# Performance work log

Hardware: AMD Instinct MI355X
Metric: run time of the kernel (lower is better)

The kernel has to match this reference:

```python
import jax, jax.numpy as jnp
import numpy as np

EPS = 1e-10
BLOCK = 8


def _block_rfft2(x):
    # x: (N, 1, H, W) -> real/imag coeffs (N, K, 8, 5), matching torch.rfft(signal_ndim=2)/b**2
    N, C, H, W = x.shape
    b = BLOCK
    Hb, Wb = H // b, W // b
    # non-overlapping 8x8 blocks, row-major over (Hb, Wb) like nn.Unfold with stride=blocksize
    blocks = x[:, 0].reshape(N, Hb, b, Wb, b).transpose(0, 1, 3, 2, 4).reshape(N, Hb * Wb, b, b)
    c = jnp.fft.rfft2(blocks) / (b * b)  # (N, K, 8, 5) complex
    return jnp.real(c).astype(x.dtype), jnp.imag(c).astype(x.dtype)


def _soft_combine(a, b):
    # softmax-weighted blend of a and b along a virtual last axis (factor=1)
    stacked = jnp.stack([a, b], axis=-1)
    f = jax.nn.softmax(stacked, axis=-1)
    return a * f[..., 0] + b * f[..., 1]


def setup_inputs() -> dict:
    key = jax.random.key(0)
    k1, k2 = jax.random.split(key)
    N, H, W = 64, 512, 512
    inp = {
        "input": jax.random.normal(k1, (N, 1, H, W), dtype=jnp.float32),
        "target": jax.random.normal(k2, (N, 1, H, W), dtype=jnp.float32),
        # learned parameters at their init values (weight_size = (8, 5))
        "t_tild": jnp.zeros((BLOCK, BLOCK // 2 + 1), dtype=jnp.float32),
        "alpha": jnp.float32(0.1),
        "w_tild": jnp.float32(np.log(0.2 / 0.8)),
        "beta": jnp.float32(1.0),
        "w_phase_tild": jnp.zeros((BLOCK, BLOCK // 2 + 1), dtype=jnp.float32) - 2.0,
    }
    return inp


def reference(input, target, t_tild, alpha, w_tild, beta, w_phase_tild):
    # blockwise 2D rFFT of both images
    c0r, c0i = _block_rfft2(target)  # (N, K, 8, 5)
    c1r, c1i = _block_rfft2(input)

    # amplitude: frobenius norm over (real, imag) after +EPS, as in torch.norm(c0+EPS, dim=4)
    c0_amp = jnp.sqrt((c0r + EPS) ** 2 + (c0i + EPS) ** 2)
    c1_amp = jnp.sqrt((c1r + EPS) ** 2 + (c1i + EPS) ** 2)

    avg_lum = jnp.mean(c0_amp[:, :, 0, 0])
    t = jnp.exp(t_tild)  # (8, 5)
    lum = ((c0_amp[:, :, 0, 0] + EPS) / (avg_lum + EPS)) ** alpha  # (N, K)
    t_l = t[None, None, :, :] * lum[:, :, None, None]  # (N, K, 8, 5)

    w = jax.nn.sigmoid(w_tild)
    s = _soft_combine(t_l, (jnp.abs(c0_amp) + EPS) ** w * t_l ** (1 - w))

    # Watson amplitude distance (dropout in eval mode = identity)
    watson = (jnp.abs((c0_amp - c1_amp) / s) + EPS) ** beta + EPS
    watson = jnp.sum(watson, axis=(1, 2, 3)) ** (1.0 / beta)  # (N,)

    # phase distance
    c0_phase = jnp.arctan2(c0i, c0r + EPS)
    c1_phase = jnp.arctan2(c1i, c1r + EPS)
    w_phase = jnp.exp(w_phase_tild)  # trainable=True branch: no corner zeroing
    phase_dist = jnp.arccos(jnp.cos(c0_phase - c1_phase) * (1 - EPS * 1e3)) * w_phase
    phase_dist = jnp.sum(phase_dist, axis=(1, 2, 3))  # (N,)

    return watson + phase_dist  # reduction='none' -> (N,)
```

## Files before the change

kernel.cpp:

```cpp
#include <hip/hip_runtime.h>
#include <math.h>

#define EPSf 1e-10f
#define IMG_N 64
#define IMG_H 512
#define IMG_W 512
#define KBLK 4096
#define TOTAL_BLK (IMG_N * KBLK)
#define WG 256
#define NWG (TOTAL_BLK / WG)
#define NWG2 (TOTAL_BLK * 2 / WG)
#define CHUNKS 32

#define KCc 0.70710678118654752440f
#define SCc (1.0f / 64.0f)
#define LOG2E 1.44269504088896340736f

#define FSQRT(x) __builtin_amdgcn_sqrtf(x)
#define FRCP(x)  __builtin_amdgcn_rcpf(x)

__device__ __forceinline__ float dpp_xor1(float x) {
    int i = __builtin_bit_cast(int, x);
    i = __builtin_amdgcn_mov_dpp(i, 0xB1, 0xF, 0xF, true);
    return __builtin_bit_cast(float, i);
}

__device__ __forceinline__ float wave_red(float v) {
#pragma unroll
    for (int o = 32; o > 0; o >>= 1) v += __shfl_down(v, o, 64);
    return v;
}

__global__ __launch_bounds__(WG) void kA(const float* __restrict__ tgt,
                                         float* __restrict__ partA) {
    int gid = blockIdx.x * WG + threadIdx.x;
    int n = gid >> 12;
    int k = gid & 4095;
    int bi = k >> 6, bj = k & 63;
    const float* p = tgt + (size_t)n * (IMG_H * IMG_W) + (size_t)(bi * 8) * IMG_W + bj * 8;
    float s = 0.f;
#pragma unroll
    for (int r = 0; r < 8; r++) {
        float4 a = *(const float4*)(p + (size_t)r * IMG_W);
        float4 b = *(const float4*)(p + (size_t)r * IMG_W + 4);
        s += ((a.x + a.y) + (a.z + a.w)) + ((b.x + b.y) + (b.z + b.w));
    }
    float dc = s * (1.0f / 64.0f);
    float amp = sqrtf((dc + EPSf) * (dc + EPSf) + EPSf * EPSf);
    float wv = wave_red(amp);
    __shared__ float red[4];
    if ((threadIdx.x & 63) == 0) red[threadIdx.x >> 6] = wv;
    __syncthreads();
    if (threadIdx.x == 0) partA[blockIdx.x] = (red[0] + red[1]) + (red[2] + red[3]);
}

#define ROWFFT(A, B, P) do { \
    float s02 = (A).x + (B).x, d02 = (A).x - (B).x; \
    float s26 = (A).z + (B).z, d26 = (A).z - (B).z; \
    float s13 = (A).y + (B).y, d13 = (A).y - (B).y; \
    float s37 = (A).w + (B).w, d37 = (A).w - (B).w; \
    float e0 = s02 + s26, e2 = s02 - s26; \
    float o0 = s13 + s37, o2 = s13 - s37; \
    float cp = KCc * (d13 - d37), cm = KCc * (d13 + d37); \
    P##_0 = SCc * (e0 + o0);  P##_1 = SCc * (d02 + cp); \
    P##_2 = SCc * (-d26 - cm); P##_3 = SCc * e2; \
    P##_4 = SCc * (-o2);      P##_5 = SCc * (d02 - cp); \
    P##_6 = SCc * (d26 - cm); P##_7 = SCc * (e0 - o0); \
} while (0)

#define DECL8(P) float P##_0, P##_1, P##_2, P##_3, P##_4, P##_5, P##_6, P##_7

#define LOADROW(ptr, r, P) do { \
    float4 A = *(const float4*)((ptr) + (size_t)(r) * IMG_W); \
    float4 B = *(const float4*)((ptr) + (size_t)(r) * IMG_W + 4); \
    ROWFFT(A, B, P); \
} while (0)

#define CFFT8M(PFX, x0r,x0i,x1r,x1i,x2r,x2i,x3r,x3i,x4r,x4i,x5r,x5i,x6r,x6i,x7r,x7i) \
    float PFX##0r, PFX##0i, PFX##1r, PFX##1i, PFX##2r, PFX##2i, PFX##3r, PFX##3i, \
          PFX##4r, PFX##4i, PFX##5r, PFX##5i, PFX##6r, PFX##6i, PFX##7r, PFX##7i; \
    { \
        float t0r = (x0r) + (x4r), t0i = (x0i) + (x4i); \
        float t1r = (x0r) - (x4r), t1i = (x0i) - (x4i); \
        float t2r = (x2r) + (x6r), t2i = (x2i) + (x6i); \
        float t3r = (x2r) - (x6r), t3i = (x2i) - (x6i); \
        float E0r = t0r + t2r, E0i = t0i + t2i; \
        float E2r = t0r - t2r, E2i = t0i - t2i; \
        float E1r = t1r + t3i, E1i = t1i - t3r; \
        float E3r = t1r - t3i, E3i = t1i + t3r; \
        float u0r = (x1r) + (x5r), u0i = (x1i) + (x5i); \
        float u1r = (x1r) - (x5r), u1i = (x1i) - (x5i); \
        float u2r = (x3r) + (x7r), u2i = (x3i) + (x7i); \
        float u3r = (x3r) - (x7r), u3i = (x3i) - (x7i); \
        float O0r = u0r + u2r, O0i = u0i + u2i; \
        float O2r = u0r - u2r, O2i = u0i - u2i; \
        float O1r = u1r + u3i, O1i = u1i - u3r; \
        float O3r = u1r - u3i, O3i = u1i + u3r; \
        float W1r = KCc * (O1r + O1i), W1i = KCc * (O1i - O1r); \
        float W2r = O2i,               W2i = -O2r; \
        float W3r = KCc * (O3i - O3r), W3i = -KCc * (O3r + O3i); \
        PFX##0r = E0r + O0r; PFX##0i = E0i + O0i; \
        PFX##1r = E1r + W1r; PFX##1i = E1i + W1i; \
        PFX##2r = E2r + W2r; PFX##2i = E2i + W2i; \
        PFX##3r = E3r + W3r; PFX##3i = E3i + W3i; \
        PFX##4r = E0r - O0r; PFX##4i = E0i - O0i; \
        PFX##5r = E1r - W1r; PFX##5i = E1i - W1i; \
        PFX##6r = E2r - W2r; PFX##6i = E2i - W2i; \
        PFX##7r = E3r - W3r; PFX##7i = E3i - W3i; \
    }

__device__ __attribute__((noinline)) float2
coef2x2(float oRA, float oIA, float rRA, float rIA, float tA, float lA, float pA,
        float oRB, float oIB, float rRB, float rIB, float tB, float lB, float pB,
        float lum, float omw_llum, float w, float beta, int img, int b1i) {
    float oReA = oRA + EPSf, oIeA = oIA + EPSf;
    float rReA = rRA + EPSf, rIeA = rIA + EPSf;
    float oReB = oRB + EPSf, oIeB = oIB + EPSf;
    float rReB = rRB + EPSf, rIeB = rIB + EPSf;
    float aOA = FSQRT(fmaf(oReA, oReA, oIeA * oIeA));
    float aRA = FSQRT(fmaf(rReA, rReA, rIeA * rIeA));
    float aOB = FSQRT(fmaf(oReB, oReB, oIeB * oIeB));
    float aRB = FSQRT(fmaf(rReB, rReB, rIeB * rIeB));
    float a0A = img ? aRA : aOA;
    float a0B = img ? aRB : aOB;
    float dxA = fabsf(aOA - aRA);
    float dxB = fabsf(aOB - aRB);
    float l0A = __log2f(a0A + EPSf);
    float l0B = __log2f(a0B + EPSf);
    float bbA = exp2f(fmaf(w, l0A, lA + omw_llum));
    float bbB = exp2f(fmaf(w, l0B, lB + omw_llum));
    float tlA = tA * lum;
    float tlB = tB * lum;
    float eA = __expf(bbA - tlA);
    float eB = __expf(bbB - tlB);
    float xA = dxA * (1.f + eA) * FRCP(fmaf(bbA, eA, tlA));
    float xB = dxB * (1.f + eB) * FRCP(fmaf(bbB, eB, tlB));
    float dwA = b1i ? xA : (__powf(xA + EPSf, beta) + EPSf);
    float dwB = b1i ? xB : (__powf(xB + EPSf, beta) + EPSf);
    float dotA = fmaf(oReA, rReA, oIA * rIA);
    float dotB = fmaf(oReB, rReB, oIB * rIB);
    float cdA = dotA * FRCP(fmaxf(aOA * aRA, 1e-30f)) * (1.f - 1e-7f);
    float cdB = dotB * FRCP(fmaxf(aOB * aRB, 1e-30f)) * (1.f - 1e-7f);
    cdA = fminf(fmaxf(cdA, -1.f), 1.f);
    cdB = fminf(fmaxf(cdB, -1.f), 1.f);
    float tA2 = fabsf(cdA), tB2 = fabsf(cdB);
    float rA2 = FSQRT(1.f - tA2), rB2 = FSQRT(1.f - tB2);
    float plA = fmaf(fmaf(fmaf(-0.0187293f, tA2, 0.0742610f), tA2, -0.2121144f), tA2, 1.5707288f);
    float plB = fmaf(fmaf(fmaf(-0.0187293f, tB2, 0.0742610f), tB2, -0.2121144f), tB2, 1.5707288f);
    float acA = rA2 * plA;
    float acB = rB2 * plB;
    acA = (cdA < 0.f) ? (3.14159265358979f - acA) : acA;
    acB = (cdB < 0.f) ? (3.14159265358979f - acB) : acB;
    return make_float2(dwA + dwB, fmaf(acA, pA, acB * pB));
}

#define PAIRC2(QA, LAr, LAi, HAr, HAi, QB, LBr, LBi, HBr, HBi) do { \
    float sAr = img ? (LAr) : (HAr), sAi = img ? (LAi) : (HAi); \
    float rAr = dpp_xor1(sAr), rAi = dpp_xor1(sAi); \
    float oAr = img ? (HAr) : (LAr), oAi = img ? (HAi) : (LAi); \
    float sBr = img ? (LBr) : (HBr), sBi = img ? (LBi) : (HBi); \
    float rBr = dpp_xor1(sBr), rBi = dpp_xor1(sBi); \
    float oBr = img ? (HBr) : (LBr), oBi = img ? (HBi) : (LBi); \
    float2 dwp = coef2x2(oAr, oAi, rAr, rAi, (QA).x, (QA).y, (QA).z, \
                         oBr, oBi, rBr, rBi, (QB).x, (QB).y, (QB).z, \
                         lum, omw_llum, w, beta, img, b1i); \
    sumW += dwp.x; sumP += dwp.y; \
} while (0)

#define PREFQ(V) \
    float4 q0 = tab4[base20 + 0 * 5 + (V)]; \
    float4 q1 = tab4[base20 + 1 * 5 + (V)]; \
    float4 q2 = tab4[base20 + 2 * 5 + (V)]; \
    float4 q3 = tab4[base20 + 3 * 5 + (V)];

#define COEFS2() do { \
    PAIRC2(q0, X0r, X0i, X4r, X4i, q1, X1r, X1i, X5r, X5i); \
    PAIRC2(q2, X2r, X2i, X6r, X6i, q3, X3r, X3i, X7r, X7i); \
} while (0)

__global__ __launch_bounds__(WG, 4) void kC(const float* __restrict__ tgt,
                                            const float* __restrict__ inp,
                                            const float* __restrict__ t_tild,
                                            const float* __restrict__ alphaP,
                                            const float* __restrict__ wtP,
                                            const float* __restrict__ betaP,
                                            const float* __restrict__ wptP,
                                            const float* __restrict__ partA,
                                            float* __restrict__ partW,
                                            float* __restrict__ partP) {
    __shared__ float4 tab4[40];
    __shared__ float redA[4];
    float w = 1.f / (1.f + __expf(-wtP[0]));
    if (threadIdx.x < 40) {
        float tt = t_tild[threadIdx.x];
        tab4[threadIdx.x] = make_float4(__expf(tt), (1.f - w) * tt * LOG2E,
                                        __expf(wptP[threadIdx.x]), 0.f);
    }
    {
        float v = partA[threadIdx.x] + partA[threadIdx.x + 256] +
                  partA[threadIdx.x + 512] + partA[threadIdx.x + 768];
        float wv = wave_red(v);
        if ((threadIdx.x & 63) == 0) redA[threadIdx.x >> 6] = wv;
    }
    __syncthreads();
    float avg = ((redA[0] + redA[1]) + (redA[2] + redA[3])) * (1.0f / (float)TOTAL_BLK);
    float alpha = alphaP[0];
    float beta = betaP[0];
    float lavg = __log2f(avg + EPSf);
    int b1i = (beta == 1.0f) ? 1 : 0;

    int gid = blockIdx.x * WG + threadIdx.x;
    int p = gid >> 1;
    int img = gid & 1;
    int base20 = img * 20;
    int n = p >> 12, k = p & 4095;
    int bi = k >> 6, bj = k & 63;
    size_t off = (size_t)n * (IMG_H * IMG_W) + (size_t)(bi * 8) * IMG_W + bj * 8;
    const float* src = (img ? inp : tgt) + off;

    DECL8(t0); DECL8(t1); DECL8(t2); DECL8(t3);
    DECL8(t4); DECL8(t5); DECL8(t6); DECL8(t7);
    LOADROW(src, 0, t0); LOADROW(src, 1, t1); LOADROW(src, 2, t2); LOADROW(src, 3, t3);
    LOADROW(src, 4, t4); LOADROW(src, 5, t5); LOADROW(src, 6, t6); LOADROW(src, 7, t7);

    float sumW = 0.f, sumP = 0.f;
    float lum = 0.f, omw_llum = 0.f;

    {
        PREFQ(0)
        CFFT8M(X, t0_0, 0.f, t1_0, 0.f, t2_0, 0.f, t3_0, 0.f,
                  t4_0, 0.f, t5_0, 0.f, t6_0, 0.f, t7_0, 0.f)
        float rr = X0r + EPSf, ii = X0i + EPSf;
        float myamp = FSQRT(fmaf(rr, rr, ii * ii));
        float oamp = dpp_xor1(myamp);
        float amp00 = img ? oamp : myamp;
        float llum = alpha * (__log2f(amp00 + EPSf) - lavg);
        lum = exp2f(llum);
        omw_llum = (1.f - w) * llum;
        COEFS2();
    }
    {
        PREFQ(1)
        CFFT8M(X, t0_1, t0_2, t1_1, t1_2, t2_1, t2_2, t3_1, t3_2,
                  t4_1, t4_2, t5_1, t5_2, t6_1, t6_2, t7_1, t7_2)
        COEFS2();
    }
    {
        PREFQ(2)
        CFFT8M(X, t0_3, t0_4, t1_3, t1_4, t2_3, t2_4, t3_3, t3_4,
                  t4_3, t4_4, t5_3, t5_4, t6_3, t6_4, t7_3, t7_4)
        COEFS2();
    }
    {
        PREFQ(3)
        CFFT8M(X, t0_5, t0_6, t1_5, t1_6, t2_5, t2_6, t3_5, t3_6,
                  t4_5, t4_6, t5_5, t5_6, t6_5, t6_6, t7_5, t7_6)
        COEFS2();
    }
    {
        PREFQ(4)
        CFFT8M(X, t0_7, 0.f, t1_7, 0.f, t2_7, 0.f, t3_7, 0.f,
                  t4_7, 0.f, t5_7, 0.f, t6_7, 0.f, t7_7, 0.f)
        COEFS2();
    }

    if (b1i) sumW += 20.f * 2.f * EPSf;

    float wW = wave_red(sumW);
    float wP = wave_red(sumP);
    __shared__ float redW[4], redP[4];
    if ((threadIdx.x & 63) == 0) { redW[threadIdx.x >> 6] = wW; redP[threadIdx.x >> 6] = wP; }
    __syncthreads();
    if (threadIdx.x == 0) {
        partW[blockIdx.x] = (redW[0] + redW[1]) + (redW[2] + redW[3]);
        partP[blockIdx.x] = (redP[0] + redP[1]) + (redP[2] + redP[3]);
    }
}

__global__ __launch_bounds__(64) void kD(const float* __restrict__ partW,
                                         const float* __restrict__ partP,
                                         const float* __restrict__ betaP,
                                         float* __restrict__ out) {
    int n = threadIdx.x;
    float sW = 0.f, sP = 0.f;
#pragma unroll
    for (int c = 0; c < CHUNKS; c++) {
        sW += partW[n * CHUNKS + c];
        sP += partP[n * CHUNKS + c];
    }
    float beta = betaP[0];
    float wat = (beta == 1.0f) ? sW : __powf(sW, 1.0f / beta);
    out[n] = wat + sP;
}

extern "C" void kernel_launch(void* const* d_in, const int* in_sizes, int n_in,
                              void* d_out, int out_size, void* d_ws, size_t ws_size,
                              hipStream_t stream) {
    const float* inp    = (const float*)d_in[0];
    const float* tgt    = (const float*)d_in[1];
    const float* t_tild = (const float*)d_in[2];
    const float* alphaP = (const float*)d_in[3];
    const float* wtP    = (const float*)d_in[4];
    const float* betaP  = (const float*)d_in[5];
    const float* wptP   = (const float*)d_in[6];
    float* out = (float*)d_out;
    float* ws = (float*)d_ws;
    float* partA = ws;
    float* partW = ws + 1056;
    float* partP = ws + 3104;

    hipLaunchKernelGGL(kA, dim3(NWG), dim3(WG), 0, stream, tgt, partA);
    hipLaunchKernelGGL(kC, dim3(NWG2), dim3(WG), 0, stream, tgt, inp, t_tild,
                       alphaP, wtP, betaP, wptP, partA, partW, partP);
    hipLaunchKernelGGL(kD, dim3(1), dim3(64), 0, stream, partW, partP, betaP, out);
}
```

Baseline: 45.85 us.

## Fuse final reduction into kC via last-block atomic counter, tweak occupancy and log

Removes the separate kD launch: kC blocks increment a global counter after writing partials, and the last block reduces the partials and writes the output. The counter is reset in kA. The amplitude log is now computed from the squared magnitude (half log2 of mag²), which drops the +EPS inside the log, and kC's launch bounds are raised to 5 waves per EU. The aim is to save a kernel launch and a little ALU work. In exchange it adds an atomic and a fence per block, and may increase register pressure or cause spills.

```diff
diff --git a/kernel.cpp b/kernel.cpp
--- a/kernel.cpp
+++ b/kernel.cpp
@@ -32,7 +32,9 @@
 }
 
 __global__ __launch_bounds__(WG) void kA(const float* __restrict__ tgt,
-                                         float* __restrict__ partA) {
+                                         float* __restrict__ partA,
+                                         unsigned int* __restrict__ cnt) {
+    if (blockIdx.x == 0 && threadIdx.x == 0) cnt[0] = 0u;
     int gid = blockIdx.x * WG + threadIdx.x;
     int n = gid >> 12;
     int k = gid & 4095;
@@ -117,16 +119,16 @@
     float rReA = rRA + EPSf, rIeA = rIA + EPSf;
     float oReB = oRB + EPSf, oIeB = oIB + EPSf;
     float rReB = rRB + EPSf, rIeB = rIB + EPSf;
-    float aOA = FSQRT(fmaf(oReA, oReA, oIeA * oIeA));
-    float aRA = FSQRT(fmaf(rReA, rReA, rIeA * rIeA));
-    float aOB = FSQRT(fmaf(oReB, oReB, oIeB * oIeB));
-    float aRB = FSQRT(fmaf(rReB, rReB, rIeB * rIeB));
-    float a0A = img ? aRA : aOA;
-    float a0B = img ? aRB : aOB;
+    float mOA = fmaf(oReA, oReA, oIeA * oIeA);
+    float mRA = fmaf(rReA, rReA, rIeA * rIeA);
+    float mOB = fmaf(oReB, oReB, oIeB * oIeB);
+    float mRB = fmaf(rReB, rReB, rIeB * rIeB);
+    float aOA = FSQRT(mOA), aRA = FSQRT(mRA);
+    float aOB = FSQRT(mOB), aRB = FSQRT(mRB);
+    float l0A = 0.5f * __log2f(img ? mRA : mOA);
+    float l0B = 0.5f * __log2f(img ? mRB : mOB);
     float dxA = fabsf(aOA - aRA);
     float dxB = fabsf(aOB - aRB);
-    float l0A = __log2f(a0A + EPSf);
-    float l0B = __log2f(a0B + EPSf);
     float bbA = exp2f(fmaf(w, l0A, lA + omw_llum));
     float bbB = exp2f(fmaf(w, l0B, lB + omw_llum));
     float tlA = tA * lum;
@@ -178,7 +180,7 @@
     PAIRC2(q2, X2r, X2i, X6r, X6i, q3, X3r, X3i, X7r, X7i); \
 } while (0)
 
-__global__ __launch_bounds__(WG, 4) void kC(const float* __restrict__ tgt,
+__global__ __launch_bounds__(WG, 5) void kC(const float* __restrict__ tgt,
                                             const float* __restrict__ inp,
                                             const float* __restrict__ t_tild,
                                             const float* __restrict__ alphaP,
@@ -187,9 +189,12 @@
                                             const float* __restrict__ wptP,
                                             const float* __restrict__ partA,
                                             float* __restrict__ partW,
-                                            float* __restrict__ partP) {
+                                            float* __restrict__ partP,
+                                            unsigned int* __restrict__ cnt,
+                                            float* __restrict__ out) {
     __shared__ float4 tab4[40];
     __shared__ float redA[4];
+    __shared__ unsigned int lastS;
     float w = 1.f / (1.f + __expf(-wtP[0]));
     if (threadIdx.x < 40) {
         float tt = t_tild[threadIdx.x];
@@ -274,23 +279,25 @@
     if (threadIdx.x == 0) {
         partW[blockIdx.x] = (redW[0] + redW[1]) + (redW[2] + redW[3]);
         partP[blockIdx.x] = (redP[0] + redP[1]) + (redP[2] + redP[3]);
-    }
-}
-
-__global__ __launch_bounds__(64) void kD(const float* __restrict__ partW,
-                                         const float* __restrict__ partP,
-                                         const float* __restrict__ betaP,
-                                         float* __restrict__ out) {
-    int n = threadIdx.x;
-    float sW = 0.f, sP = 0.f;
+        __threadfence();
+        unsigned int c = atomicAdd(cnt, 1u);
+        lastS = (c == (unsigned int)(NWG2 - 1)) ? 1u : 0u;
+    }
+    __syncthreads();
+    if (lastS) {
+        __threadfence();
+        if (threadIdx.x < IMG_N) {
+            int nn = threadIdx.x;
+            float sW = 0.f, sP = 0.f;
 #pragma unroll
-    for (int c = 0; c < CHUNKS; c++) {
-        sW += partW[n * CHUNKS + c];
-        sP += partP[n * CHUNKS + c];
-    }
-    float beta = betaP[0];
-    float wat = (beta == 1.0f) ? sW : __powf(sW, 1.0f / beta);
-    out[n] = wat + sP;
+            for (int c = 0; c < CHUNKS; c++) {
+                sW += partW[nn * CHUNKS + c];
+                sP += partP[nn * CHUNKS + c];
+            }
+            float wat = b1i ? sW : __powf(sW, 1.0f / beta);
+            out[nn] = wat + sP;
+        }
+    }
 }
 
 extern "C" void kernel_launch(void* const* d_in, const int* in_sizes, int n_in,
@@ -306,11 +313,11 @@
     float* out = (float*)d_out;
     float* ws = (float*)d_ws;
     float* partA = ws;
+    unsigned int* cnt = (unsigned int*)(ws + 1040);
     float* partW = ws + 1056;
     float* partP = ws + 3104;
 
-    hipLaunchKernelGGL(kA, dim3(NWG), dim3(WG), 0, stream, tgt, partA);
+    hipLaunchKernelGGL(kA, dim3(NWG), dim3(WG), 0, stream, tgt, partA, cnt);
     hipLaunchKernelGGL(kC, dim3(NWG2), dim3(WG), 0, stream, tgt, inp, t_tild,
-                       alphaP, wtP, betaP, wptP, partA, partW, partP);
-    hipLaunchKernelGGL(kD, dim3(1), dim3(64), 0, stream, partW, partP, betaP, out);
-}
+                       alphaP, wtP, betaP, wptP, partA, partW, partP, cnt, out);
+}
```

Result: slower. 118.9 us (+159.4%).

## Split each block's column FFT across four lanes using DPP radix-2 exchange

Applied to the files above, without the earlier changes.

Each 8x8 block per image is now handled by two lanes instead of one. Each lane loads four rows (the even or odd rows), does a 4-point column FFT, and the final radix-2 butterfly is completed by exchanging partial results with a DPP xor-2 swap. The DC amplitude is broadcast from lane 0 of each quad. The grid doubles, which halves per-thread registers and work to raise parallelism and occupancy, at the cost of extra cross-lane moves, select overhead, and twice as many workgroup partials to reduce.

```diff
diff --git a/kernel.cpp b/kernel.cpp
--- a/kernel.cpp
+++ b/kernel.cpp
@@ -9,8 +9,8 @@
 #define TOTAL_BLK (IMG_N * KBLK)
 #define WG 256
 #define NWG (TOTAL_BLK / WG)
-#define NWG2 (TOTAL_BLK * 2 / WG)
-#define CHUNKS 32
+#define NWG4 (TOTAL_BLK * 4 / WG)
+#define CHUNKS 64
 
 #define KCc 0.70710678118654752440f
 #define SCc (1.0f / 64.0f)
@@ -22,6 +22,16 @@
 __device__ __forceinline__ float dpp_xor1(float x) {
     int i = __builtin_bit_cast(int, x);
     i = __builtin_amdgcn_mov_dpp(i, 0xB1, 0xF, 0xF, true);
+    return __builtin_bit_cast(float, i);
+}
+__device__ __forceinline__ float dpp_xor2(float x) {
+    int i = __builtin_bit_cast(int, x);
+    i = __builtin_amdgcn_mov_dpp(i, 0x4E, 0xF, 0xF, true);
+    return __builtin_bit_cast(float, i);
+}
+__device__ __forceinline__ float dpp_bcast0(float x) {
+    int i = __builtin_bit_cast(int, x);
+    i = __builtin_amdgcn_mov_dpp(i, 0x00, 0xF, 0xF, true);
     return __builtin_bit_cast(float, i);
 }
 
@@ -75,39 +85,6 @@
     float4 B = *(const float4*)((ptr) + (size_t)(r) * IMG_W + 4); \
     ROWFFT(A, B, P); \
 } while (0)
-
-#define CFFT8M(PFX, x0r,x0i,x1r,x1i,x2r,x2i,x3r,x3i,x4r,x4i,x5r,x5i,x6r,x6i,x7r,x7i) \
-    float PFX##0r, PFX##0i, PFX##1r, PFX##1i, PFX##2r, PFX##2i, PFX##3r, PFX##3i, \
-          PFX##4r, PFX##4i, PFX##5r, PFX##5i, PFX##6r, PFX##6i, PFX##7r, PFX##7i; \
-    { \
-        float t0r = (x0r) + (x4r), t0i = (x0i) + (x4i); \
-        float t1r = (x0r) - (x4r), t1i = (x0i) - (x4i); \
-        float t2r = (x2r) + (x6r), t2i = (x2i) + (x6i); \
-        float t3r = (x2r) - (x6r), t3i = (x2i) - (x6i); \
-        float E0r = t0r + t2r, E0i = t0i + t2i; \
-        float E2r = t0r - t2r, E2i = t0i - t2i; \
-        float E1r = t1r + t3i, E1i = t1i - t3r; \
-        float E3r = t1r - t3i, E3i = t1i + t3r; \
-        float u0r = (x1r) + (x5r), u0i = (x1i) + (x5i); \
-        float u1r = (x1r) - (x5r), u1i = (x1i) - (x5i); \
-        float u2r = (x3r) + (x7r), u2i = (x3i) + (x7i); \
-        float u3r = (x3r) - (x7r), u3i = (x3i) - (x7i); \
-        float O0r = u0r + u2r, O0i = u0i + u2i; \
-        float O2r = u0r - u2r, O2i = u0i - u2i; \
-        float O1r = u1r + u3i, O1i = u1i - u3r; \
-        float O3r = u1r - u3i, O3i = u1i + u3r; \
-        float W1r = KCc * (O1r + O1i), W1i = KCc * (O1i - O1r); \
-        float W2r = O2i,               W2i = -O2r; \
-        float W3r = KCc * (O3i - O3r), W3i = -KCc * (O3r + O3i); \
-        PFX##0r = E0r + O0r; PFX##0i = E0i + O0i; \
-        PFX##1r = E1r + W1r; PFX##1i = E1i + W1i; \
-        PFX##2r = E2r + W2r; PFX##2i = E2i + W2i; \
-        PFX##3r = E3r + W3r; PFX##3i = E3i + W3i; \
-        PFX##4r = E0r - O0r; PFX##4i = E0i - O0i; \
-        PFX##5r = E1r - W1r; PFX##5i = E1i - W1i; \
-        PFX##6r = E2r - W2r; PFX##6i = E2i - W2i; \
-        PFX##7r = E3r - W3r; PFX##7i = E3i - W3i; \
-    }
 
 __device__ __attribute__((noinline)) float2
 coef2x2(float oRA, float oIA, float rRA, float rIA, float tA, float lA, float pA,
@@ -154,28 +131,55 @@
     return make_float2(dwA + dwB, fmaf(acA, pA, acB * pB));
 }
 
-#define PAIRC2(QA, LAr, LAi, HAr, HAi, QB, LBr, LBi, HBr, HBi) do { \
-    float sAr = img ? (LAr) : (HAr), sAi = img ? (LAi) : (HAi); \
-    float rAr = dpp_xor1(sAr), rAi = dpp_xor1(sAi); \
-    float oAr = img ? (HAr) : (LAr), oAi = img ? (HAi) : (LAi); \
-    float sBr = img ? (LBr) : (HBr), sBi = img ? (LBi) : (HBi); \
-    float rBr = dpp_xor1(sBr), rBi = dpp_xor1(sBi); \
-    float oBr = img ? (HBr) : (LBr), oBi = img ? (HBi) : (LBi); \
-    float2 dwp = coef2x2(oAr, oAi, rAr, rAi, (QA).x, (QA).y, (QA).z, \
-                         oBr, oBi, rBr, rBi, (QB).x, (QB).y, (QB).z, \
+#define COLSTEP(V, a0r,a0i,a1r,a1i,a2r,a2i,a3r,a3i, ISV0) do { \
+    float4 qA = tab4[baseU5 + (V)]; \
+    float4 qB = tab4[baseU5 + 5 + (V)]; \
+    float t0r=(a0r)+(a2r), t0i=(a0i)+(a2i); \
+    float t1r=(a0r)-(a2r), t1i=(a0i)-(a2i); \
+    float t2r=(a1r)+(a3r), t2i=(a1i)+(a3i); \
+    float t3r=(a1r)-(a3r), t3i=(a1i)-(a3i); \
+    float F0r=t0r+t2r, F0i=t0i+t2i; \
+    float F1r=t1r+t3i, F1i=t1i-t3r; \
+    float F2r=t0r-t2r, F2i=t0i-t2i; \
+    float F3r=t1r-t3i, F3i=t1i+t3r; \
+    float P0r=dpp_xor2(F0r), P0i=dpp_xor2(F0i); \
+    float P1r=dpp_xor2(F1r), P1i=dpp_xor2(F1i); \
+    float P2r=dpp_xor2(F2r), P2i=dpp_xor2(F2i); \
+    float P3r=dpp_xor2(F3r), P3i=dpp_xor2(F3i); \
+    float E0r = half ? P0r : F0r, E0i = half ? P0i : F0i; \
+    float O0r = half ? F0r : P0r, O0i = half ? F0i : P0i; \
+    float E1r = half ? P1r : F1r, E1i = half ? P1i : F1i; \
+    float O1r = half ? F1r : P1r, O1i = half ? F1i : P1i; \
+    float E2r = half ? P2r : F2r, E2i = half ? P2i : F2i; \
+    float O2r = half ? F2r : P2r, O2i = half ? F2i : P2i; \
+    float E3r = half ? P3r : F3r, E3i = half ? P3i : F3i; \
+    float O3r = half ? F3r : P3r, O3i = half ? F3i : P3i; \
+    float W1r = KCc*(O1r+O1i), W1i = KCc*(O1i-O1r); \
+    float W2r = O2i,           W2i = -O2r; \
+    float W3r = KCc*(O3i-O3r), W3i = -KCc*(O3r+O3i); \
+    float X0r = fmaf(sgn, O0r, E0r), X0i = fmaf(sgn, O0i, E0i); \
+    float X1r = fmaf(sgn, W1r, E1r), X1i = fmaf(sgn, W1i, E1i); \
+    float X2r = fmaf(sgn, W2r, E2r), X2i = fmaf(sgn, W2i, E2i); \
+    float X3r = fmaf(sgn, W3r, E3r), X3i = fmaf(sgn, W3i, E3i); \
+    if (ISV0) {  \
+        float rr = X0r + EPSf, ii = X0i + EPSf; \
+        float myamp = FSQRT(fmaf(rr, rr, ii * ii)); \
+        float amp00 = dpp_bcast0(myamp); \
+        float llum = alpha * (__log2f(amp00 + EPSf) - lavg); \
+        lum = exp2f(llum); \
+        omw_llum = (1.f - w) * llum; \
+    } \
+     \
+    float s0r = img ? X0r : X2r, s0i = img ? X0i : X2i; \
+    float s1r = img ? X1r : X3r, s1i = img ? X1i : X3i; \
+    float r0r = dpp_xor1(s0r), r0i = dpp_xor1(s0i); \
+    float r1r = dpp_xor1(s1r), r1i = dpp_xor1(s1i); \
+    float oAr = img ? X2r : X0r, oAi = img ? X2i : X0i; \
+    float oBr = img ? X3r : X1r, oBi = img ? X3i : X1i; \
+    float2 dwp = coef2x2(oAr, oAi, r0r, r0i, qA.x, qA.y, qA.z, \
+                         oBr, oBi, r1r, r1i, qB.x, qB.y, qB.z, \
                          lum, omw_llum, w, beta, img, b1i); \
     sumW += dwp.x; sumP += dwp.y; \
-} while (0)
-
-#define PREFQ(V) \
-    float4 q0 = tab4[base20 + 0 * 5 + (V)]; \
-    float4 q1 = tab4[base20 + 1 * 5 + (V)]; \
-    float4 q2 = tab4[base20 + 2 * 5 + (V)]; \
-    float4 q3 = tab4[base20 + 3 * 5 + (V)];
-
-#define COEFS2() do { \
-    PAIRC2(q0, X0r, X0i, X4r, X4i, q1, X1r, X1i, X5r, X5i); \
-    PAIRC2(q2, X2r, X2i, X6r, X6i, q3, X3r, X3i, X7r, X7i); \
 } while (0)
 
 __global__ __launch_bounds__(WG, 4) void kC(const float* __restrict__ tgt,
@@ -210,61 +214,32 @@
     int b1i = (beta == 1.0f) ? 1 : 0;
 
     int gid = blockIdx.x * WG + threadIdx.x;
-    int p = gid >> 1;
+    int p = gid >> 2;
     int img = gid & 1;
-    int base20 = img * 20;
+    int half = (gid >> 1) & 1;
+    float sgn = half ? -1.f : 1.f;
+    int baseU5 = half * 20 + img * 10;
     int n = p >> 12, k = p & 4095;
     int bi = k >> 6, bj = k & 63;
     size_t off = (size_t)n * (IMG_H * IMG_W) + (size_t)(bi * 8) * IMG_W + bj * 8;
     const float* src = (img ? inp : tgt) + off;
 
-    DECL8(t0); DECL8(t1); DECL8(t2); DECL8(t3);
-    DECL8(t4); DECL8(t5); DECL8(t6); DECL8(t7);
-    LOADROW(src, 0, t0); LOADROW(src, 1, t1); LOADROW(src, 2, t2); LOADROW(src, 3, t3);
-    LOADROW(src, 4, t4); LOADROW(src, 5, t5); LOADROW(src, 6, t6); LOADROW(src, 7, t7);
+    DECL8(y0); DECL8(y1); DECL8(y2); DECL8(y3);
+    LOADROW(src, half,     y0);
+    LOADROW(src, 2 + half, y1);
+    LOADROW(src, 4 + half, y2);
+    LOADROW(src, 6 + half, y3);
 
     float sumW = 0.f, sumP = 0.f;
     float lum = 0.f, omw_llum = 0.f;
 
-    {
-        PREFQ(0)
-        CFFT8M(X, t0_0, 0.f, t1_0, 0.f, t2_0, 0.f, t3_0, 0.f,
-                  t4_0, 0.f, t5_0, 0.f, t6_0, 0.f, t7_0, 0.f)
-        float rr = X0r + EPSf, ii = X0i + EPSf;
-        float myamp = FSQRT(fmaf(rr, rr, ii * ii));
-        float oamp = dpp_xor1(myamp);
-        float amp00 = img ? oamp : myamp;
-        float llum = alpha * (__log2f(amp00 + EPSf) - lavg);
-        lum = exp2f(llum);
-        omw_llum = (1.f - w) * llum;
-        COEFS2();
-    }
-    {
-        PREFQ(1)
-        CFFT8M(X, t0_1, t0_2, t1_1, t1_2, t2_1, t2_2, t3_1, t3_2,
-                  t4_1, t4_2, t5_1, t5_2, t6_1, t6_2, t7_1, t7_2)
-        COEFS2();
-    }
-    {
-        PREFQ(2)
-        CFFT8M(X, t0_3, t0_4, t1_3, t1_4, t2_3, t2_4, t3_3, t3_4,
-                  t4_3, t4_4, t5_3, t5_4, t6_3, t6_4, t7_3, t7_4)
-        COEFS2();
-    }
-    {
-        PREFQ(3)
-        CFFT8M(X, t0_5, t0_6, t1_5, t1_6, t2_5, t2_6, t3_5, t3_6,
-                  t4_5, t4_6, t5_5, t5_6, t6_5, t6_6, t7_5, t7_6)
-        COEFS2();
-    }
-    {
-        PREFQ(4)
-        CFFT8M(X, t0_7, 0.f, t1_7, 0.f, t2_7, 0.f, t3_7, 0.f,
-                  t4_7, 0.f, t5_7, 0.f, t6_7, 0.f, t7_7, 0.f)
-        COEFS2();
-    }
-
-    if (b1i) sumW += 20.f * 2.f * EPSf;
+    COLSTEP(0, y0_0, 0.f,  y1_0, 0.f,  y2_0, 0.f,  y3_0, 0.f,  1);
+    COLSTEP(1, y0_1, y0_2, y1_1, y1_2, y2_1, y2_2, y3_1, y3_2, 0);
+    COLSTEP(2, y0_3, y0_4, y1_3, y1_4, y2_3, y2_4, y3_3, y3_4, 0);
+    COLSTEP(3, y0_5, y0_6, y1_5, y1_6, y2_5, y2_6, y3_5, y3_6, 0);
+    COLSTEP(4, y0_7, 0.f,  y1_7, 0.f,  y2_7, 0.f,  y3_7, 0.f,  0);
+
+    if (b1i) sumW += 10.f * 2.f * EPSf;
 
     float wW = wave_red(sumW);
     float wP = wave_red(sumP);
@@ -307,10 +282,10 @@
     float* ws = (float*)d_ws;
     float* partA = ws;
     float* partW = ws + 1056;
-    float* partP = ws + 3104;
+    float* partP = ws + 5152;
 
     hipLaunchKernelGGL(kA, dim3(NWG), dim3(WG), 0, stream, tgt, partA);
-    hipLaunchKernelGGL(kC, dim3(NWG2), dim3(WG), 0, stream, tgt, inp, t_tild,
+    hipLaunchKernelGGL(kC, dim3(NWG4), dim3(WG), 0, stream, tgt, inp, t_tild,
                        alphaP, wtP, betaP, wptP, partA, partW, partP);
     hipLaunchKernelGGL(kD, dim3(1), dim3(64), 0, stream, partW, partP, betaP, out);
 }
```

After: 48.67 us. 1.06x slower.
